# Kernel tuning notes

Hardware: AMD Instinct MI355X
Metric: run time of the kernel (lower is better)

The kernel has to match this reference:

```python
import jax, jax.numpy as jnp
import numpy as np

NUM_EXPERTS = 8
TOP_K = 2
B, S, H, I = 4, 2048, 2048, 1408
INIT = 0.02


def setup_inputs() -> dict:
    key = jax.random.key(0)
    ks = jax.random.split(key, 6)
    return {
        "selected_experts": jax.random.randint(ks[0], (B, S, TOP_K), 0, NUM_EXPERTS, dtype=jnp.int32),
        "hidden_states": jax.random.normal(ks[1], (B, S, H), dtype=jnp.float32),
        "routing_weights": jax.random.uniform(ks[2], (B, S, TOP_K), dtype=jnp.float32),
        "gate_w": jax.random.normal(ks[3], (NUM_EXPERTS, H, I), dtype=jnp.float32) * INIT,
        "up_w": jax.random.normal(ks[4], (NUM_EXPERTS, H, I), dtype=jnp.float32) * INIT,
        "down_w": jax.random.normal(ks[5], (NUM_EXPERTS, I, H), dtype=jnp.float32) * INIT,
        "batch_size": B,
        "sequence_length": S,
        "hidden_dim": H,
    }


def reference(selected_experts, hidden_states, routing_weights, gate_w, up_w, down_w,
              batch_size, sequence_length, hidden_dim):
    # Naive MoE: every expert's SwiGLU MLP runs on every token, then the
    # output is scaled by sum((selected_experts == e) * routing_weights, -1).
    num_experts = gate_w.shape[0]
    final = jnp.zeros_like(hidden_states)
    for e in range(num_experts):  # fixed small expert count, structurally a loop in the original
        g = jnp.einsum("bsh,hi->bsi", hidden_states, gate_w[e])
        u = jnp.einsum("bsh,hi->bsi", hidden_states, up_w[e])
        out = jnp.einsum("bsi,ih->bsh", jax.nn.silu(g) * u, down_w[e])
        w = jnp.sum(jnp.where(selected_experts == e, routing_weights, 0.0), axis=-1)  # [B,S]
        final = final + w[:, :, None] * out
    return final
```

## Files before the change

### kernel.cpp

```cpp
#include <hip/hip_runtime.h>
#include <stdint.h>

#define TT 8192
#define HH 2048
#define II 1408
#define NE 8
#define NROWS (TT*2)
#define BM 128
#define BK 64
#define MAX_SLOTS 144
#define NKT_GU (HH/BK)
#define NKT_DN (II/BK)
#define NYT_GU (II/64)
#define NYT_DN (HH/64)
#define SLOTS_PER_XCD (MAX_SLOTS/8)

typedef unsigned short u16;
typedef __attribute__((ext_vector_type(8))) __bf16 bhalf8;
typedef __attribute__((ext_vector_type(4))) float f32x4;
typedef __attribute__((ext_vector_type(4))) float float4v;
typedef __attribute__((ext_vector_type(4))) int int4v;

__device__ __forceinline__ u16 f2bf(float f) {
  union { float f; unsigned u; } v; v.f = f;
  return (u16)((v.u + 0x7FFFu + ((v.u >> 16) & 1u)) >> 16);
}

__device__ __forceinline__ void gld16(const void* g, void* l) {
  __builtin_amdgcn_global_load_lds(
      (const __attribute__((address_space(1))) unsigned int*)g,
      (__attribute__((address_space(3))) unsigned int*)l, 16, 0, 0);
}

__global__ __launch_bounds__(256) void k_cvt_hs(const float* __restrict__ in,
                                                u16* __restrict__ out) {
  size_t i = ((size_t)blockIdx.x * 256 + threadIdx.x) * 8;
  float4v a = *(const float4v*)(in + i);
  float4v b = *(const float4v*)(in + i + 4);
  u16 o[8];
  o[0] = f2bf(a.x); o[1] = f2bf(a.y); o[2] = f2bf(a.z); o[3] = f2bf(a.w);
  o[4] = f2bf(b.x); o[5] = f2bf(b.y); o[6] = f2bf(b.z); o[7] = f2bf(b.w);
  *(int4v*)(out + i) = *(const int4v*)o;
}

__global__ __launch_bounds__(256) void k_tconv(const float* __restrict__ in,
                                               u16* __restrict__ out,
                                               int R, int C) {
  __shared__ float t[64][65];
  int e = blockIdx.z;
  int r0 = blockIdx.y * 64, c0 = blockIdx.x * 64;
  const float* ip = in + (size_t)e * R * C;
  u16* op = out + (size_t)e * R * C;
  int tid = threadIdx.x;
  int rr = tid >> 4, c4 = (tid & 15) * 4;
#pragma unroll
  for (int j = 0; j < 4; ++j) {
    float4v v = *(const float4v*)&ip[(size_t)(r0 + rr + 16 * j) * C + c0 + c4];
    t[rr + 16 * j][c4 + 0] = v.x;
    t[rr + 16 * j][c4 + 1] = v.y;
    t[rr + 16 * j][c4 + 2] = v.z;
    t[rr + 16 * j][c4 + 3] = v.w;
  }
  __syncthreads();
  int cc = tid >> 2, rb = (tid & 3) * 16;
  u16 buf[16];
#pragma unroll
  for (int i = 0; i < 16; ++i) buf[i] = f2bf(t[rb + i][cc]);
  u16* p = op + (size_t)(c0 + cc) * R + r0 + rb;
  *(int4v*)p = *(const int4v*)&buf[0];
  *(int4v*)(p + 8) = *(const int4v*)&buf[8];
}

__global__ __launch_bounds__(256) void k_route(const int* __restrict__ sel,
                                               const float* __restrict__ rw,
                                               int* __restrict__ token_idx,
                                               float* __restrict__ wrow,
                                               int* __restrict__ s_e,
                                               int* __restrict__ s_rs,
                                               int* __restrict__ s_rows) {
  __shared__ int cnt[NE], offs[NE + 1], cursor[NE];
  int tid = threadIdx.x;
  if (tid < NE) cnt[tid] = 0;
  __syncthreads();
  for (int i = tid; i < NROWS; i += 256) atomicAdd(&cnt[sel[i]], 1);
  __syncthreads();
  if (tid == 0) {
    int o = 0;
    for (int e = 0; e < NE; ++e) { offs[e] = o; o += cnt[e]; }
    offs[NE] = o;
    int ns = 0;
    for (int e = 0; e < NE; ++e) {
      for (int t = 0; t < cnt[e]; t += BM) {
        s_e[ns] = e;
        s_rs[ns] = offs[e] + t;
        s_rows[ns] = (cnt[e] - t < BM) ? (cnt[e] - t) : BM;
        ns++;
      }
    }
    for (; ns < MAX_SLOTS; ++ns) s_rows[ns] = 0;
  }
  __syncthreads();
  if (tid < NE) cursor[tid] = offs[tid];
  __syncthreads();
  for (int i = tid; i < NROWS; i += 256) {
    int e = sel[i];
    int r = atomicAdd(&cursor[e], 1);
    token_idx[r] = i >> 1;
    wrow[r] = rw[i];
  }
}

__global__ __launch_bounds__(256, 4) void k_gu(const u16* __restrict__ hsb,
                                               const u16* __restrict__ gwt,
                                               const u16* __restrict__ uwt,
                                               const int* __restrict__ token_idx,
                                               const float* __restrict__ wrow,
                                               const int* __restrict__ s_e,
                                               const int* __restrict__ s_rs,
                                               const int* __restrict__ s_rows,
                                               u16* __restrict__ act) {
  int f = blockIdx.x;
  int xcd = f & 7;
  int pos = f >> 3;
  int slot = xcd * SLOTS_PER_XCD + pos / NYT_GU;
  int ytile = pos % NYT_GU;
  int nrows = s_rows[slot];
  if (nrows == 0) return;
  int e = s_e[slot];
  int row0 = s_rs[slot];
  int i0 = ytile * 64;

  __shared__ alignas(16) u16 As[BM][BK];
  __shared__ alignas(16) u16 Bg[64][BK];
  __shared__ alignas(16) u16 Bu[64][BK];

  int tid = threadIdx.x;
  int lane = tid & 63;
  int wid = tid >> 6;
  int l8 = lane >> 3;
  int c8 = lane & 7;
  int cs = c8 ^ l8;

  const u16* agp[4];
#pragma unroll
  for (int j = 0; j < 4; ++j) {
    int gr = row0 + wid * 32 + j * 8 + l8;
    if (gr > NROWS - 1) gr = NROWS - 1;
    int tok = token_idx[gr];
    agp[j] = hsb + (size_t)tok * HH + cs * 8;
  }
  const u16* ggp[2]; const u16* ugp[2];
#pragma unroll
  for (int j = 0; j < 2; ++j) {
    size_t off = ((size_t)e * II + i0 + wid * 16 + j * 8 + l8) * HH + cs * 8;
    ggp[j] = gwt + off;
    ugp[j] = uwt + off;
  }

  int wm = wid >> 1, wn = wid & 1;
  int l15 = lane & 15, l16 = lane >> 4;

  f32x4 accg[4][2], accu[4][2];
#pragma unroll
  for (int a = 0; a < 4; ++a)
#pragma unroll
    for (int b = 0; b < 2; ++b) { accg[a][b] = (f32x4)0.0f; accu[a][b] = (f32x4)0.0f; }

  for (int kt = 0; kt < NKT_GU; ++kt) {
    int k0 = kt * BK;
#pragma unroll
    for (int j = 0; j < 4; ++j) gld16(agp[j] + k0, &As[wid * 32 + j * 8][0]);
#pragma unroll
    for (int j = 0; j < 2; ++j) {
      gld16(ggp[j] + k0, &Bg[wid * 16 + j * 8][0]);
      gld16(ugp[j] + k0, &Bu[wid * 16 + j * 8][0]);
    }
    __syncthreads();
#pragma unroll
    for (int ks = 0; ks < 2; ++ks) {
      bhalf8 af[4], bgf[2], buf_[2];
#pragma unroll
      for (int mf = 0; mf < 4; ++mf) {
        int row = wm * 64 + mf * 16 + l15;
        int c = (ks * 4 + l16) ^ (row & 7);
        af[mf] = *(const bhalf8*)&As[row][c * 8];
      }
#pragma unroll
      for (int nf = 0; nf < 2; ++nf) {
        int row = wn * 32 + nf * 16 + l15;
        int c = (ks * 4 + l16) ^ (row & 7);
        bgf[nf] = *(const bhalf8*)&Bg[row][c * 8];
        buf_[nf] = *(const bhalf8*)&Bu[row][c * 8];
      }
#pragma unroll
      for (int mf = 0; mf < 4; ++mf)
#pragma unroll
        for (int nf = 0; nf < 2; ++nf) {
          accg[mf][nf] = __builtin_amdgcn_mfma_f32_16x16x32_bf16(af[mf], bgf[nf], accg[mf][nf], 0, 0, 0);
          accu[mf][nf] = __builtin_amdgcn_mfma_f32_16x16x32_bf16(af[mf], buf_[nf], accu[mf][nf], 0, 0, 0);
        }
    }
    __syncthreads();
  }

#pragma unroll
  for (int mf = 0; mf < 4; ++mf) {
#pragma unroll
    for (int j = 0; j < 4; ++j) {
      int lm = wm * 64 + mf * 16 + l16 * 4 + j;
      if (lm < nrows) {
        int gr = row0 + lm;
        float w = wrow[gr];
        size_t base = (size_t)gr * II + i0 + wn * 32 + l15;
#pragma unroll
        for (int nf = 0; nf < 2; ++nf) {
          float g = accg[mf][nf][j];
          float u = accu[mf][nf][j];
          float s = g / (1.0f + __expf(-g));
          act[base + nf * 16] = f2bf(s * u * w);
        }
      }
    }
  }
}

__global__ __launch_bounds__(256, 4) void k_down(const u16* __restrict__ act,
                                                 const u16* __restrict__ dwt,
                                                 const int* __restrict__ token_idx,
                                                 const int* __restrict__ s_e,
                                                 const int* __restrict__ s_rs,
                                                 const int* __restrict__ s_rows,
                                                 float* __restrict__ out) {
  int f = blockIdx.x;
  int xcd = f & 7;
  int pos = f >> 3;
  int slot = xcd * SLOTS_PER_XCD + pos / NYT_DN;
  int ytile = pos % NYT_DN;
  int nrows = s_rows[slot];
  if (nrows == 0) return;
  int e = s_e[slot];
  int row0 = s_rs[slot];
  int h0 = ytile * 64;

  __shared__ alignas(16) u16 As[BM][BK];
  __shared__ alignas(16) u16 Bs[64][BK];

  int tid = threadIdx.x;
  int lane = tid & 63;
  int wid = tid >> 6;
  int l8 = lane >> 3;
  int c8 = lane & 7;
  int cs = c8 ^ l8;

  const u16* agp[4];
#pragma unroll
  for (int j = 0; j < 4; ++j) {
    int gr = row0 + wid * 32 + j * 8 + l8;
    if (gr > NROWS - 1) gr = NROWS - 1;
    agp[j] = act + (size_t)gr * II + cs * 8;
  }
  const u16* bgp[2];
#pragma unroll
  for (int j = 0; j < 2; ++j)
    bgp[j] = dwt + ((size_t)e * HH + h0 + wid * 16 + j * 8 + l8) * II + cs * 8;

  int wm = wid >> 1, wn = wid & 1;
  int l15 = lane & 15, l16 = lane >> 4;

  f32x4 acc[4][2];
#pragma unroll
  for (int a = 0; a < 4; ++a)
#pragma unroll
    for (int b = 0; b < 2; ++b) acc[a][b] = (f32x4)0.0f;

  for (int kt = 0; kt < NKT_DN; ++kt) {
    int k0 = kt * BK;
#pragma unroll
    for (int j = 0; j < 4; ++j) gld16(agp[j] + k0, &As[wid * 32 + j * 8][0]);
#pragma unroll
    for (int j = 0; j < 2; ++j) gld16(bgp[j] + k0, &Bs[wid * 16 + j * 8][0]);
    __syncthreads();
#pragma unroll
    for (int ks = 0; ks < 2; ++ks) {
      bhalf8 af[4], bf[2];
#pragma unroll
      for (int mf = 0; mf < 4; ++mf) {
        int row = wm * 64 + mf * 16 + l15;
        int c = (ks * 4 + l16) ^ (row & 7);
        af[mf] = *(const bhalf8*)&As[row][c * 8];
      }
#pragma unroll
      for (int nf = 0; nf < 2; ++nf) {
        int row = wn * 32 + nf * 16 + l15;
        int c = (ks * 4 + l16) ^ (row & 7);
        bf[nf] = *(const bhalf8*)&Bs[row][c * 8];
      }
#pragma unroll
      for (int mf = 0; mf < 4; ++mf)
#pragma unroll
        for (int nf = 0; nf < 2; ++nf)
          acc[mf][nf] = __builtin_amdgcn_mfma_f32_16x16x32_bf16(af[mf], bf[nf], acc[mf][nf], 0, 0, 0);
    }
    __syncthreads();
  }

#pragma unroll
  for (int mf = 0; mf < 4; ++mf) {
#pragma unroll
    for (int j = 0; j < 4; ++j) {
      int lm = wm * 64 + mf * 16 + l16 * 4 + j;
      if (lm < nrows) {
        int tok = token_idx[row0 + lm];
        size_t base = (size_t)tok * HH + h0 + wn * 32 + l15;
#pragma unroll
        for (int nf = 0; nf < 2; ++nf)
          atomicAdd(&out[base + nf * 16], acc[mf][nf][j]);
      }
    }
  }
}

extern "C" void kernel_launch(void* const* d_in, const int* in_sizes, int n_in,
                              void* d_out, int out_size, void* d_ws, size_t ws_size,
                              hipStream_t stream) {
  const int* sel = (const int*)d_in[0];
  const float* hs = (const float*)d_in[1];
  const float* rw = (const float*)d_in[2];
  const float* gw = (const float*)d_in[3];
  const float* uw = (const float*)d_in[4];
  const float* dw = (const float*)d_in[5];
  float* out = (float*)d_out;

  char* ws = (char*)d_ws;
  size_t o = 0;
  u16* hsb = (u16*)(ws + o); o += (size_t)TT * HH * 2;
  u16* gwt = (u16*)(ws + o); o += (size_t)NE * HH * II * 2;
  u16* uwt = (u16*)(ws + o); o += (size_t)NE * HH * II * 2;
  u16* dwt = (u16*)(ws + o); o += (size_t)NE * HH * II * 2;
  u16* act = (u16*)(ws + o); o += (size_t)NROWS * II * 2;
  int* token_idx = (int*)(ws + o); o += (size_t)NROWS * 4;
  float* wrow = (float*)(ws + o); o += (size_t)NROWS * 4;
  int* s_e = (int*)(ws + o); o += MAX_SLOTS * 4;
  int* s_rs = (int*)(ws + o); o += MAX_SLOTS * 4;
  int* s_rows = (int*)(ws + o); o += MAX_SLOTS * 4;
  (void)ws_size; (void)in_sizes; (void)n_in; (void)out_size;

  k_cvt_hs<<<(TT * HH) / 2048, 256, 0, stream>>>(hs, hsb);
  dim3 g1(II / 64, HH / 64, NE);
  k_tconv<<<g1, 256, 0, stream>>>(gw, gwt, HH, II);
  k_tconv<<<g1, 256, 0, stream>>>(uw, uwt, HH, II);
  dim3 g2(HH / 64, II / 64, NE);
  k_tconv<<<g2, 256, 0, stream>>>(dw, dwt, II, HH);

  k_route<<<1, 256, 0, stream>>>(sel, rw, token_idx, wrow, s_e, s_rs, s_rows);
  hipMemsetAsync(d_out, 0, (size_t)TT * HH * 4, stream);

  k_gu<<<MAX_SLOTS * NYT_GU, 256, 0, stream>>>(hsb, gwt, uwt, token_idx, wrow,
                                               s_e, s_rs, s_rows, act);

  k_down<<<MAX_SLOTS * NYT_DN, 256, 0, stream>>>(act, dwt, token_idx,
                                                 s_e, s_rs, s_rows, out);
}
```

Before: 574.7 us.

## Double-buffer LDS tiles in gate/up and down GEMM kernels

Both expert GEMM kernels now keep two shared-memory buffers per operand. The next K tile is issued into the spare buffer before the MFMA work on the current tile runs, so global-to-LDS loads overlap compute instead of stalling behind a barrier. This doubles LDS use per block, so the launch-bounds occupancy hints drop to 2 blocks per CU for gate/up and 3 for down. Fewer resident waves could cost latency hiding from other blocks.

```diff
diff --git a/kernel.cpp b/kernel.cpp
--- a/kernel.cpp
+++ b/kernel.cpp
@@ -110,7 +110,7 @@
   }
 }
 
-__global__ __launch_bounds__(256, 4) void k_gu(const u16* __restrict__ hsb,
+__global__ __launch_bounds__(256, 2) void k_gu(const u16* __restrict__ hsb,
                                                const u16* __restrict__ gwt,
                                                const u16* __restrict__ uwt,
                                                const int* __restrict__ token_idx,
@@ -130,9 +130,9 @@
   int row0 = s_rs[slot];
   int i0 = ytile * 64;
 
-  __shared__ alignas(16) u16 As[BM][BK];
-  __shared__ alignas(16) u16 Bg[64][BK];
-  __shared__ alignas(16) u16 Bu[64][BK];
+  __shared__ alignas(16) u16 As[2][BM][BK];
+  __shared__ alignas(16) u16 Bg[2][64][BK];
+  __shared__ alignas(16) u16 Bu[2][64][BK];
 
   int tid = threadIdx.x;
   int lane = tid & 63;
@@ -166,16 +166,22 @@
 #pragma unroll
     for (int b = 0; b < 2; ++b) { accg[a][b] = (f32x4)0.0f; accu[a][b] = (f32x4)0.0f; }
 
+  auto stage = [&](int b, int k0) {
+#pragma unroll
+    for (int j = 0; j < 4; ++j) gld16(agp[j] + k0, &As[b][wid * 32 + j * 8][0]);
+#pragma unroll
+    for (int j = 0; j < 2; ++j) {
+      gld16(ggp[j] + k0, &Bg[b][wid * 16 + j * 8][0]);
+      gld16(ugp[j] + k0, &Bu[b][wid * 16 + j * 8][0]);
+    }
+  };
+
+  stage(0, 0);
+  __syncthreads();
+
   for (int kt = 0; kt < NKT_GU; ++kt) {
-    int k0 = kt * BK;
-#pragma unroll
-    for (int j = 0; j < 4; ++j) gld16(agp[j] + k0, &As[wid * 32 + j * 8][0]);
-#pragma unroll
-    for (int j = 0; j < 2; ++j) {
-      gld16(ggp[j] + k0, &Bg[wid * 16 + j * 8][0]);
-      gld16(ugp[j] + k0, &Bu[wid * 16 + j * 8][0]);
-    }
-    __syncthreads();
+    int cur = kt & 1;
+    if (kt + 1 < NKT_GU) stage(cur ^ 1, (kt + 1) * BK);
 #pragma unroll
     for (int ks = 0; ks < 2; ++ks) {
       bhalf8 af[4], bgf[2], buf_[2];
@@ -183,14 +189,14 @@
       for (int mf = 0; mf < 4; ++mf) {
         int row = wm * 64 + mf * 16 + l15;
         int c = (ks * 4 + l16) ^ (row & 7);
-        af[mf] = *(const bhalf8*)&As[row][c * 8];
+        af[mf] = *(const bhalf8*)&As[cur][row][c * 8];
       }
 #pragma unroll
       for (int nf = 0; nf < 2; ++nf) {
         int row = wn * 32 + nf * 16 + l15;
         int c = (ks * 4 + l16) ^ (row & 7);
-        bgf[nf] = *(const bhalf8*)&Bg[row][c * 8];
-        buf_[nf] = *(const bhalf8*)&Bu[row][c * 8];
+        bgf[nf] = *(const bhalf8*)&Bg[cur][row][c * 8];
+        buf_[nf] = *(const bhalf8*)&Bu[cur][row][c * 8];
       }
 #pragma unroll
       for (int mf = 0; mf < 4; ++mf)
@@ -224,7 +230,7 @@
   }
 }
 
-__global__ __launch_bounds__(256, 4) void k_down(const u16* __restrict__ act,
+__global__ __launch_bounds__(256, 3) void k_down(const u16* __restrict__ act,
                                                  const u16* __restrict__ dwt,
                                                  const int* __restrict__ token_idx,
                                                  const int* __restrict__ s_e,
@@ -242,8 +248,8 @@
   int row0 = s_rs[slot];
   int h0 = ytile * 64;
 
-  __shared__ alignas(16) u16 As[BM][BK];
-  __shared__ alignas(16) u16 Bs[64][BK];
+  __shared__ alignas(16) u16 As[2][BM][BK];
+  __shared__ alignas(16) u16 Bs[2][64][BK];
 
   int tid = threadIdx.x;
   int lane = tid & 63;
@@ -273,13 +279,19 @@
 #pragma unroll
     for (int b = 0; b < 2; ++b) acc[a][b] = (f32x4)0.0f;
 
+  auto stage = [&](int b, int k0) {
+#pragma unroll
+    for (int j = 0; j < 4; ++j) gld16(agp[j] + k0, &As[b][wid * 32 + j * 8][0]);
+#pragma unroll
+    for (int j = 0; j < 2; ++j) gld16(bgp[j] + k0, &Bs[b][wid * 16 + j * 8][0]);
+  };
+
+  stage(0, 0);
+  __syncthreads();
+
   for (int kt = 0; kt < NKT_DN; ++kt) {
-    int k0 = kt * BK;
-#pragma unroll
-    for (int j = 0; j < 4; ++j) gld16(agp[j] + k0, &As[wid * 32 + j * 8][0]);
-#pragma unroll
-    for (int j = 0; j < 2; ++j) gld16(bgp[j] + k0, &Bs[wid * 16 + j * 8][0]);
-    __syncthreads();
+    int cur = kt & 1;
+    if (kt + 1 < NKT_DN) stage(cur ^ 1, (kt + 1) * BK);
 #pragma unroll
     for (int ks = 0; ks < 2; ++ks) {
       bhalf8 af[4], bf[2];
@@ -287,13 +299,13 @@
       for (int mf = 0; mf < 4; ++mf) {
         int row = wm * 64 + mf * 16 + l15;
         int c = (ks * 4 + l16) ^ (row & 7);
-        af[mf] = *(const bhalf8*)&As[row][c * 8];
+        af[mf] = *(const bhalf8*)&As[cur][row][c * 8];
       }
 #pragma unroll
       for (int nf = 0; nf < 2; ++nf) {
         int row = wn * 32 + nf * 16 + l15;
         int c = (ks * 4 + l16) ^ (row & 7);
-        bf[nf] = *(const bhalf8*)&Bs[row][c * 8];
+        bf[nf] = *(const bhalf8*)&Bs[cur][row][c * 8];
       }
 #pragma unroll
       for (int mf = 0; mf < 4; ++mf)
```

Result: slower. 687.5 us (+19.6%).

## Widen down-projection N tile to 128 and merge gate/up weight conversion launches

Applied to the files above, without the earlier changes.

The down-projection kernel now computes a 128x128 output tile per block instead of 128x64. Each A tile of activations is reused across twice as many output columns, which halves the number of blocks and the repeated activation loads. The cost is more accumulator registers, and launch bounds drop to 3 blocks per SM to allow for them. Separately, the gate and up weight transpose/convert passes are fused into a single launch through the z grid dimension, saving one kernel launch.

```diff
diff --git a/kernel.cpp b/kernel.cpp
--- a/kernel.cpp
+++ b/kernel.cpp
@@ -8,12 +8,13 @@
 #define NROWS (TT*2)
 #define BM 128
 #define BK 64
+#define BND 128
 #define MAX_SLOTS 144
 #define NKT_GU (HH/BK)
 #define NKT_DN (II/BK)
 #define NYT_GU (II/64)
-#define NYT_DN (HH/64)
-#define SLOTS_PER_XCD (MAX_SLOTS/8)
+#define NYT_DN (HH/BND)
+#define SPX (MAX_SLOTS/8)
 
 typedef unsigned short u16;
 typedef __attribute__((ext_vector_type(8))) __bf16 bhalf8;
@@ -48,6 +49,39 @@
                                                int R, int C) {
   __shared__ float t[64][65];
   int e = blockIdx.z;
+  int r0 = blockIdx.y * 64, c0 = blockIdx.x * 64;
+  const float* ip = in + (size_t)e * R * C;
+  u16* op = out + (size_t)e * R * C;
+  int tid = threadIdx.x;
+  int rr = tid >> 4, c4 = (tid & 15) * 4;
+#pragma unroll
+  for (int j = 0; j < 4; ++j) {
+    float4v v = *(const float4v*)&ip[(size_t)(r0 + rr + 16 * j) * C + c0 + c4];
+    t[rr + 16 * j][c4 + 0] = v.x;
+    t[rr + 16 * j][c4 + 1] = v.y;
+    t[rr + 16 * j][c4 + 2] = v.z;
+    t[rr + 16 * j][c4 + 3] = v.w;
+  }
+  __syncthreads();
+  int cc = tid >> 2, rb = (tid & 3) * 16;
+  u16 buf[16];
+#pragma unroll
+  for (int i = 0; i < 16; ++i) buf[i] = f2bf(t[rb + i][cc]);
+  u16* p = op + (size_t)(c0 + cc) * R + r0 + rb;
+  *(int4v*)p = *(const int4v*)&buf[0];
+  *(int4v*)(p + 8) = *(const int4v*)&buf[8];
+}
+
+__global__ __launch_bounds__(256) void k_tconv2(const float* __restrict__ gw,
+                                                const float* __restrict__ uw,
+                                                u16* __restrict__ gwt,
+                                                u16* __restrict__ uwt) {
+  __shared__ float t[64][65];
+  const int R = HH, C = II;
+  int z = blockIdx.z;
+  int e = z & 7;
+  const float* in = (z < 8) ? gw : uw;
+  u16* out = (z < 8) ? gwt : uwt;
   int r0 = blockIdx.y * 64, c0 = blockIdx.x * 64;
   const float* ip = in + (size_t)e * R * C;
   u16* op = out + (size_t)e * R * C;
@@ -122,7 +156,7 @@
   int f = blockIdx.x;
   int xcd = f & 7;
   int pos = f >> 3;
-  int slot = xcd * SLOTS_PER_XCD + pos / NYT_GU;
+  int slot = xcd * SPX + pos / NYT_GU;
   int ytile = pos % NYT_GU;
   int nrows = s_rows[slot];
   if (nrows == 0) return;
@@ -224,7 +258,7 @@
   }
 }
 
-__global__ __launch_bounds__(256, 4) void k_down(const u16* __restrict__ act,
+__global__ __launch_bounds__(256, 3) void k_down(const u16* __restrict__ act,
                                                  const u16* __restrict__ dwt,
                                                  const int* __restrict__ token_idx,
                                                  const int* __restrict__ s_e,
@@ -234,16 +268,16 @@
   int f = blockIdx.x;
   int xcd = f & 7;
   int pos = f >> 3;
-  int slot = xcd * SLOTS_PER_XCD + pos / NYT_DN;
+  int slot = xcd * SPX + pos / NYT_DN;
   int ytile = pos % NYT_DN;
   int nrows = s_rows[slot];
   if (nrows == 0) return;
   int e = s_e[slot];
   int row0 = s_rs[slot];
-  int h0 = ytile * 64;
+  int h0 = ytile * BND;
 
   __shared__ alignas(16) u16 As[BM][BK];
-  __shared__ alignas(16) u16 Bs[64][BK];
+  __shared__ alignas(16) u16 Bs[BND][BK];
 
   int tid = threadIdx.x;
   int lane = tid & 63;
@@ -259,30 +293,31 @@
     if (gr > NROWS - 1) gr = NROWS - 1;
     agp[j] = act + (size_t)gr * II + cs * 8;
   }
-  const u16* bgp[2];
-#pragma unroll
-  for (int j = 0; j < 2; ++j)
-    bgp[j] = dwt + ((size_t)e * HH + h0 + wid * 16 + j * 8 + l8) * II + cs * 8;
+  const u16* bgp[4];
+#pragma unroll
+  for (int j = 0; j < 4; ++j)
+    bgp[j] = dwt + ((size_t)e * HH + h0 + wid * 32 + j * 8 + l8) * II + cs * 8;
 
   int wm = wid >> 1, wn = wid & 1;
   int l15 = lane & 15, l16 = lane >> 4;
 
-  f32x4 acc[4][2];
+  f32x4 acc[4][4];
 #pragma unroll
   for (int a = 0; a < 4; ++a)
 #pragma unroll
-    for (int b = 0; b < 2; ++b) acc[a][b] = (f32x4)0.0f;
+    for (int b = 0; b < 4; ++b) acc[a][b] = (f32x4)0.0f;
 
   for (int kt = 0; kt < NKT_DN; ++kt) {
     int k0 = kt * BK;
 #pragma unroll
-    for (int j = 0; j < 4; ++j) gld16(agp[j] + k0, &As[wid * 32 + j * 8][0]);
-#pragma unroll
-    for (int j = 0; j < 2; ++j) gld16(bgp[j] + k0, &Bs[wid * 16 + j * 8][0]);
+    for (int j = 0; j < 4; ++j) {
+      gld16(agp[j] + k0, &As[wid * 32 + j * 8][0]);
+      gld16(bgp[j] + k0, &Bs[wid * 32 + j * 8][0]);
+    }
     __syncthreads();
 #pragma unroll
     for (int ks = 0; ks < 2; ++ks) {
-      bhalf8 af[4], bf[2];
+      bhalf8 af[4], bf[4];
 #pragma unroll
       for (int mf = 0; mf < 4; ++mf) {
         int row = wm * 64 + mf * 16 + l15;
@@ -290,15 +325,15 @@
         af[mf] = *(const bhalf8*)&As[row][c * 8];
       }
 #pragma unroll
-      for (int nf = 0; nf < 2; ++nf) {
-        int row = wn * 32 + nf * 16 + l15;
+      for (int nf = 0; nf < 4; ++nf) {
+        int row = wn * 64 + nf * 16 + l15;
         int c = (ks * 4 + l16) ^ (row & 7);
         bf[nf] = *(const bhalf8*)&Bs[row][c * 8];
       }
 #pragma unroll
       for (int mf = 0; mf < 4; ++mf)
 #pragma unroll
-        for (int nf = 0; nf < 2; ++nf)
+        for (int nf = 0; nf < 4; ++nf)
           acc[mf][nf] = __builtin_amdgcn_mfma_f32_16x16x32_bf16(af[mf], bf[nf], acc[mf][nf], 0, 0, 0);
     }
     __syncthreads();
@@ -311,9 +346,9 @@
       int lm = wm * 64 + mf * 16 + l16 * 4 + j;
       if (lm < nrows) {
         int tok = token_idx[row0 + lm];
-        size_t base = (size_t)tok * HH + h0 + wn * 32 + l15;
-#pragma unroll
-        for (int nf = 0; nf < 2; ++nf)
+        size_t base = (size_t)tok * HH + h0 + wn * 64 + l15;
+#pragma unroll
+        for (int nf = 0; nf < 4; ++nf)
           atomicAdd(&out[base + nf * 16], acc[mf][nf][j]);
       }
     }
@@ -346,9 +381,8 @@
   (void)ws_size; (void)in_sizes; (void)n_in; (void)out_size;
 
   k_cvt_hs<<<(TT * HH) / 2048, 256, 0, stream>>>(hs, hsb);
-  dim3 g1(II / 64, HH / 64, NE);
-  k_tconv<<<g1, 256, 0, stream>>>(gw, gwt, HH, II);
-  k_tconv<<<g1, 256, 0, stream>>>(uw, uwt, HH, II);
+  dim3 g1(II / 64, HH / 64, 2 * NE);
+  k_tconv2<<<g1, 256, 0, stream>>>(gw, uw, gwt, uwt);
   dim3 g2(HH / 64, II / 64, NE);
   k_tconv<<<g2, 256, 0, stream>>>(dw, dwt, II, HH);
 
```

After: 566.9 us. About the same (-1.4%).
